# Performance work log

Hardware: AMD Instinct MI355X
Metric: run time of the kernel (lower is better)

## Reference

```python
import jax, jax.numpy as jnp
import numpy as np

B, S, D, H, FF = 16, 384, 768, 12, 3072
DH = D // H


def layer_norm(x, g, b, eps=1e-5):
    m = jnp.mean(x, axis=-1, keepdims=True)
    v = jnp.mean((x - m) ** 2, axis=-1, keepdims=True)
    return (x - m) * jax.lax.rsqrt(v + eps) * g + b


def setup_inputs() -> dict:
    key = jax.random.key(0)
    ks = jax.random.split(key, 12)
    s = 0.02
    return {
        "x": jax.random.normal(ks[0], (B, S, D), dtype=jnp.float32),
        "pe": jax.random.normal(ks[1], (2 * S - 1, D), dtype=jnp.float32) * s,  # relative-position table for offsets -(S-1)..(S-1)
        "Wq": jax.random.normal(ks[2], (D, D), dtype=jnp.float32) * s,
        "Wk": jax.random.normal(ks[3], (D, D), dtype=jnp.float32) * s,
        "Wv": jax.random.normal(ks[4], (D, D), dtype=jnp.float32) * s,
        "Wr": jax.random.normal(ks[5], (D, D), dtype=jnp.float32) * s,
        "u": jax.random.normal(ks[6], (H, DH), dtype=jnp.float32) * s,  # content bias (Transformer-XL)
        "v": jax.random.normal(ks[7], (H, DH), dtype=jnp.float32) * s,  # position bias
        "Wo": jax.random.normal(ks[8], (D, D), dtype=jnp.float32) * s,  # attn_ff output projection
        "ln1_g": jnp.ones((D,), dtype=jnp.float32),
        "ln1_b": jnp.zeros((D,), dtype=jnp.float32),
        "ln2_g": jnp.ones((D,), dtype=jnp.float32),
        "ln2_b": jnp.zeros((D,), dtype=jnp.float32),
        "W1": jax.random.normal(ks[9], (D, FF), dtype=jnp.float32) * s,
        "b1": jnp.zeros((FF,), dtype=jnp.float32),
        "W2": jax.random.normal(ks[10], (FF, D), dtype=jnp.float32) * s,
        "b2": jnp.zeros((D,), dtype=jnp.float32),
    }


def reference(x, pe, Wq, Wk, Wv, Wr, u, v, Wo, ln1_g, ln1_b, ln2_g, ln2_b, W1, b1, W2, b2):
    # --- relative-position multi-head self-attention (FLAT / Transformer-XL style) ---
    q = (x @ Wq).reshape(B, S, H, DH)
    k = (x @ Wk).reshape(B, S, H, DH)
    val = (x @ Wv).reshape(B, S, H, DH)
    # project relative table once, then gather per (i, j) offset
    r = (pe @ Wr).reshape(2 * S - 1, H, DH)
    idx = jnp.arange(S)[:, None] - jnp.arange(S)[None, :] + (S - 1)  # [S,S], offset i-j shifted
    rel = r[idx]  # [S,S,H,DH]
    A_C = jnp.einsum("bqhd,bkhd->bhqk", q + u, k)
    B_D = jnp.einsum("bqhd,qkhd->bhqk", q + v, rel)
    scores = (A_C + B_D) * (1.0 / np.sqrt(DH))  # scaled=True
    p = jax.nn.softmax(scores, axis=-1)
    attn = jnp.einsum("bhqk,bkhd->bqhd", p, val).reshape(B, S, D) @ Wo
    # layer_postprocess_sequence = 'an': add residual, then layernorm
    x1 = layer_norm(x + attn, ln1_g, ln1_b)
    # --- FFN (relu) with 'an' postprocess ---
    ff = jax.nn.relu(x1 @ W1 + b1) @ W2 + b2
    return layer_norm(x1 + ff, ln2_g, ln2_b)
```

## Files before the change

kernel.cpp:

```cpp
#include <hip/hip_runtime.h>

typedef unsigned short u16;
typedef __attribute__((ext_vector_type(8))) short short8;
typedef __attribute__((ext_vector_type(4))) float floatx4;

#define B_  16
#define S_  384
#define D_  768
#define H_  12
#define DH_ 64
#define FF_ 3072

__device__ __forceinline__ float b2f(u16 h) { return __uint_as_float(((unsigned)h) << 16); }
__device__ __forceinline__ u16 f2b(float f) {
  unsigned u = __float_as_uint(f);
  u += 0x7fffu + ((u >> 16) & 1u);
  return (u16)(u >> 16);
}

__device__ __forceinline__ void gload16(const u16* g, u16* l) {
  __builtin_amdgcn_global_load_lds(
      (const __attribute__((address_space(1))) unsigned int*)g,
      (__attribute__((address_space(3))) unsigned int*)l, 16, 0, 0);
}

__global__ __launch_bounds__(256) void fill_sentinel(u16* out, int n) {
  int i = blockIdx.x * 256 + threadIdx.x;
  if (i < n) out[i] = 0x42DE;
}

__global__ __launch_bounds__(256) void detect_dtype(const u16* __restrict__ x, int* flag) {
  __shared__ int cnt;
  if (threadIdx.x == 0) cnt = 0;
  __syncthreads();
  int c = 0;
  for (int i = threadIdx.x; i < 8192; i += 256) {
    const unsigned e = (x[i] >> 7) & 0xFFu;
    if (e >= 0xC0u) ++c;
  }
  atomicAdd(&cnt, c);
  __syncthreads();
  if (threadIdx.x == 0) *flag = (cnt > 64) ? 1 : 0;
}

__global__ __launch_bounds__(256) void convert_in4(const void* __restrict__ src,
                                                   u16* __restrict__ dst, int n4,
                                                   const int* __restrict__ flag) {
  const int i = blockIdx.x * 256 + threadIdx.x;
  if (i >= n4) return;
  if (*flag) {
    const float4 f = ((const float4*)src)[i];
    ushort4 o;
    o.x = f2b(f.x); o.y = f2b(f.y); o.z = f2b(f.z); o.w = f2b(f.w);
    ((ushort4*)dst)[i] = o;
  } else {
    ((ushort4*)dst)[i] = ((const ushort4*)src)[i];
  }
}

__global__ __launch_bounds__(256) void convert_small(
    const void* b1, const void* ub, const void* vb, const void* b2,
    const void* g1, const void* be1, const void* g2, const void* be2,
    u16* b1c, u16* ubc, u16* vbc, u16* b2c,
    u16* g1c, u16* be1c, u16* g2c, u16* be2c, const int* __restrict__ flag) {
  const int i = blockIdx.x * 256 + threadIdx.x;
  if (i >= 8448) return;
  const void* s; u16* d; int off;
  if (i < 3072) { s = b1; d = b1c; off = i; }
  else {
    const int r = i - 3072, sg = r / 768; off = r - sg * 768;
    switch (sg) {
      case 0: s = ub;  d = ubc;  break;
      case 1: s = vb;  d = vbc;  break;
      case 2: s = b2;  d = b2c;  break;
      case 3: s = g1;  d = g1c;  break;
      case 4: s = be1; d = be1c; break;
      case 5: s = g2;  d = g2c;  break;
      default: s = be2; d = be2c; break;
    }
  }
  d[off] = (*flag) ? f2b(((const float*)s)[off]) : ((const u16*)s)[off];
}

struct TP { const void* src[7]; u16* dst[7]; };
__global__ __launch_bounds__(256) void transpose_all(TP tp, const int* __restrict__ flag) {
  __shared__ u16 t[32][33];
  const int f32 = *flag;
  const int id = blockIdx.x;
  int w, tt, R, C, bc, br;
  if (id < 2880)      { w = id / 576; tt = id % 576;  R = 768;  C = 768;  bc = (tt % 24) * 32; br = (tt / 24) * 32; }
  else if (id < 5184) { w = 5;        tt = id - 2880; R = 768;  C = 3072; bc = (tt % 96) * 32; br = (tt / 96) * 32; }
  else                { w = 6;        tt = id - 5184; R = 3072; C = 768;  bc = (tt % 24) * 32; br = (tt / 24) * 32; }
  const void* in = tp.src[w];
  u16* out = tp.dst[w];
  const int tx = threadIdx.x & 31, ty = threadIdx.x >> 5;
  for (int i = ty; i < 32; i += 8) {
    const size_t idx = (size_t)(br + i) * C + bc + tx;
    t[i][tx] = f32 ? f2b(((const float*)in)[idx]) : ((const u16*)in)[idx];
  }
  __syncthreads();
  for (int i = ty; i < 32; i += 8) out[(size_t)(bc + i) * R + br + tx] = t[tx][i];
}

enum { F_BIAS = 1, F_RELU = 2, F_RES = 4, F_QKV = 8 };

template <int TM, int TN, int WM, int WN, int FLAGS>
__global__ __launch_bounds__(256) void gemm3(
    const u16* __restrict__ A, const u16* __restrict__ Bt,
    u16* __restrict__ out0, u16* __restrict__ out1,
    u16* __restrict__ out2, u16* __restrict__ out3,
    const u16* __restrict__ bias0, const u16* __restrict__ bias1,
    const u16* __restrict__ res, int M, int N, int K) {
  constexpr int WAVES_M = TM / WM;
  constexpr int MT = WM / 16, NT = WN / 16;
  constexpr int NI = (TM + TN) / 64;
  static_assert((TM / WM) * (TN / WN) == 4, "4 waves");
  __shared__ u16 SM[2][(TM + TN) * 32];

  const int m0 = blockIdx.y * TM;
  const int n0 = blockIdx.x * TN;
  const int tid = threadIdx.x;
  const int wid = tid >> 6, lane = tid & 63;
  const int wm = (wid % WAVES_M) * WM, wn = (wid / WAVES_M) * WN;
  const int lm = lane & 15, quad = lane >> 4;

  floatx4 acc[MT][NT];
#pragma unroll
  for (int i = 0; i < MT; ++i)
#pragma unroll
    for (int j = 0; j < NT; ++j) acc[i][j] = (floatx4){0.f, 0.f, 0.f, 0.f};

  const u16* srcs[NI];
  int ldso[NI];
#pragma unroll
  for (int i = 0; i < NI; ++i) {
    const int j = wid + 4 * i;
    const int r = j * 16 + (lane >> 2);
    const int q = (lane & 3) ^ ((r >> 1) & 3);
    const u16* p;
    if (r < TM) {
      int ga = m0 + r;
      if (ga > M - 1) ga = M - 1;
      p = A + (size_t)ga * K + q * 8;
    } else {
      p = Bt + (size_t)(n0 + r - TM) * K + q * 8;
    }
    srcs[i] = p;
    ldso[i] = j * 512;
  }
  const int slot = (quad ^ ((lm >> 1) & 3)) * 8;
  int aoff[MT], boff[NT];
#pragma unroll
  for (int t = 0; t < MT; ++t) aoff[t] = (wm + t * 16 + lm) * 32 + slot;
#pragma unroll
  for (int t = 0; t < NT; ++t) boff[t] = (TM + wn + t * 16 + lm) * 32 + slot;

#pragma unroll
  for (int i = 0; i < NI; ++i) gload16(srcs[i], &SM[0][ldso[i]]);
  __syncthreads();

  int buf = 0;
  for (int k0 = 0; k0 < K; k0 += 32, buf ^= 1) {
    if (k0 + 32 < K) {
      const int koff = (k0 + 32);
#pragma unroll
      for (int i = 0; i < NI; ++i) gload16(srcs[i] + koff, &SM[buf ^ 1][ldso[i]]);
    }
    short8 af[MT], bf[NT];
#pragma unroll
    for (int t = 0; t < MT; ++t) af[t] = *(const short8*)(&SM[buf][aoff[t]]);
#pragma unroll
    for (int t = 0; t < NT; ++t) bf[t] = *(const short8*)(&SM[buf][boff[t]]);
#pragma unroll
    for (int tm = 0; tm < MT; ++tm)
#pragma unroll
      for (int tn = 0; tn < NT; ++tn)
        acc[tm][tn] = __builtin_amdgcn_mfma_f32_16x16x32_bf16(af[tm], bf[tn], acc[tm][tn], 0, 0, 0);
    __syncthreads();
  }

#pragma unroll
  for (int tm = 0; tm < MT; ++tm) {
#pragma unroll
    for (int tn = 0; tn < NT; ++tn) {
      const int gcol = n0 + wn + tn * 16 + lm;
#pragma unroll
      for (int r = 0; r < 4; ++r) {
        const int grow = m0 + wm + tm * 16 + quad * 4 + r;
        if (grow >= M) continue;
        float val = acc[tm][tn][r];
        if (FLAGS & F_QKV) {
          const int region = gcol / 768;
          const int c = gcol - region * 768;
          if (region == 0) {
            out0[(size_t)grow * 768 + c] = f2b(val + b2f(bias0[c]));
            out1[(size_t)grow * 768 + c] = f2b(val + b2f(bias1[c]));
          } else if (region == 1) {
            out2[(size_t)grow * 768 + c] = f2b(val);
          } else {
            const int bb = grow / S_, s = grow - bb * S_;
            out3[((size_t)bb * D_ + c) * S_ + s] = f2b(val);
          }
        } else {
          if (FLAGS & F_BIAS) val += b2f(bias0[gcol]);
          if (FLAGS & F_RES) val += b2f(res[(size_t)grow * N + gcol]);
          if (FLAGS & F_RELU) val = fmaxf(val, 0.f);
          out0[(size_t)grow * N + gcol] = f2b(val);
        }
      }
    }
  }
}

__global__ __launch_bounds__(256) void attn_kernel(
    const u16* __restrict__ qu, const u16* __restrict__ qv,
    const u16* __restrict__ kb, const u16* __restrict__ vt,
    const u16* __restrict__ rb, u16* __restrict__ attn) {
  __shared__ float scA[16 * 388];
  __shared__ float E[16 * 404];
  __shared__ float rsum[16];

  const int id = blockIdx.x;
  const int g = id >> 3;
  const int qt = g % 24;
  const int bh = (id & 7) + 8 * (g / 24);
  const int b = bh / H_, h = bh % H_;
  const int i0 = qt * 16;
  const int tid = threadIdx.x, wid = tid >> 6, lane = tid & 63;
  const int lm = lane & 15, quad = lane >> 4;

  const size_t qrow = ((size_t)(b * S_ + i0 + lm)) * D_ + h * DH_;
  {
    const short8 a0 = *(const short8*)(qv + qrow + quad * 8);
    const short8 a1 = *(const short8*)(qv + qrow + 32 + quad * 8);
    for (int tt = wid; tt < 25; tt += 4) {
      const int trel = tt * 16 + lm;
      int t = i0 + trel;
      if (t > 766) t = 766;
      const size_t rrow = (size_t)t * D_ + h * DH_;
      const short8 b0 = *(const short8*)(rb + rrow + quad * 8);
      const short8 b1 = *(const short8*)(rb + rrow + 32 + quad * 8);
      floatx4 e = (floatx4){0.f, 0.f, 0.f, 0.f};
      e = __builtin_amdgcn_mfma_f32_16x16x32_bf16(a0, b0, e, 0, 0, 0);
      e = __builtin_amdgcn_mfma_f32_16x16x32_bf16(a1, b1, e, 0, 0, 0);
#pragma unroll
      for (int r = 0; r < 4; ++r) E[(quad * 4 + r) * 404 + trel] = e[r];
    }
  }
  {
    const short8 a0 = *(const short8*)(qu + qrow + quad * 8);
    const short8 a1 = *(const short8*)(qu + qrow + 32 + quad * 8);
    for (int q = 0; q < 6; ++q) {
      const int j0 = (wid * 6 + q) * 16;
      const size_t krow = ((size_t)(b * S_ + j0 + lm)) * D_ + h * DH_;
      const short8 b0 = *(const short8*)(kb + krow + quad * 8);
      const short8 b1 = *(const short8*)(kb + krow + 32 + quad * 8);
      floatx4 e = (floatx4){0.f, 0.f, 0.f, 0.f};
      e = __builtin_amdgcn_mfma_f32_16x16x32_bf16(a0, b0, e, 0, 0, 0);
      e = __builtin_amdgcn_mfma_f32_16x16x32_bf16(a1, b1, e, 0, 0, 0);
#pragma unroll
      for (int r = 0; r < 4; ++r) scA[(quad * 4 + r) * 388 + j0 + lm] = e[r];
    }
  }
  __syncthreads();

  u16* p16 = (u16*)scA;
  {
    const int row = wid * 4 + quad;
    float v[24];
    float lmax = -1e30f;
#pragma unroll
    for (int cc = 0; cc < 24; ++cc) {
      const int c = lm + cc * 16;
      const float s = (scA[row * 388 + c] + E[row * 404 + row + 383 - c]) * 0.125f;
      v[cc] = s;
      lmax = fmaxf(lmax, s);
    }
#pragma unroll
    for (int m = 1; m < 16; m <<= 1) lmax = fmaxf(lmax, __shfl_xor(lmax, m));
    float lsum = 0.f;
#pragma unroll
    for (int cc = 0; cc < 24; ++cc) {
      const float e = __expf(v[cc] - lmax);
      p16[row * 776 + lm + cc * 16] = f2b(e);
      lsum += e;
    }
#pragma unroll
    for (int m = 1; m < 16; m <<= 1) lsum += __shfl_xor(lsum, m);
    if (lm == 0) rsum[row] = lsum;
  }
  __syncthreads();

  floatx4 o[4];
#pragma unroll
  for (int nt = 0; nt < 4; ++nt) o[nt] = (floatx4){0.f, 0.f, 0.f, 0.f};
  for (int kk = 0; kk < 3; ++kk) {
    const int kbase = wid * 96 + kk * 32;
    const short8 af = *(const short8*)(&p16[lm * 776 + kbase + quad * 8]);
#pragma unroll
    for (int nt = 0; nt < 4; ++nt) {
      const size_t vrow = ((size_t)(b * D_ + h * DH_ + nt * 16 + lm)) * S_;
      const short8 bv = *(const short8*)(vt + vrow + kbase + quad * 8);
      o[nt] = __builtin_amdgcn_mfma_f32_16x16x32_bf16(af, bv, o[nt], 0, 0, 0);
    }
  }
#pragma unroll
  for (int nt = 0; nt < 4; ++nt)
#pragma unroll
    for (int r = 0; r < 4; ++r)
      E[wid * 1088 + (quad * 4 + r) * 68 + nt * 16 + lm] = o[nt][r];
  __syncthreads();

#pragma unroll
  for (int i = 0; i < 4; ++i) {
    const int idx = tid + 256 * i;
    const int row = idx >> 6, dh = idx & 63;
    float v = E[row * 68 + dh] + E[1088 + row * 68 + dh] +
              E[2176 + row * 68 + dh] + E[3264 + row * 68 + dh];
    v /= rsum[row];
    attn[((size_t)(b * S_ + i0 + row)) * D_ + h * DH_ + dh] = f2b(v);
  }
}

__global__ __launch_bounds__(256) void ln_kernel(const u16* __restrict__ y,
                                                 const u16* __restrict__ g,
                                                 const u16* __restrict__ bb,
                                                 void* __restrict__ outv,
                                                 const int* __restrict__ flag, int dual) {
  const int row = blockIdx.x * 4 + (threadIdx.x >> 6);
  const int lane = threadIdx.x & 63;
  const u16* yr = y + (size_t)row * D_;
  float vbuf[12], s = 0.f, s2 = 0.f;
#pragma unroll
  for (int i = 0; i < 12; ++i) {
    const float x = b2f(yr[lane + i * 64]);
    vbuf[i] = x;
    s += x;
    s2 += x * x;
  }
#pragma unroll
  for (int off = 32; off; off >>= 1) {
    s += __shfl_down(s, off);
    s2 += __shfl_down(s2, off);
  }
  s = __shfl(s, 0);
  s2 = __shfl(s2, 0);
  const float mean = s * (1.f / 768.f);
  const float var = s2 * (1.f / 768.f) - mean * mean;
  const float inv = rsqrtf(var + 1e-5f);
  const int f32out = dual && *flag;
#pragma unroll
  for (int i = 0; i < 12; ++i) {
    const int c = lane + i * 64;
    const float val = (vbuf[i] - mean) * inv * b2f(g[c]) + b2f(bb[c]);
    if (f32out) ((float*)outv)[(size_t)row * D_ + c] = val;
    else ((u16*)outv)[(size_t)row * D_ + c] = f2b(val);
  }
}

extern "C" void kernel_launch(void* const* d_in, const int* in_sizes, int n_in,
                              void* d_out, int out_size, void* d_ws, size_t ws_size,
                              hipStream_t stream) {
  const void* x    = d_in[0];
  const void* pe   = d_in[1];
  const void* Wq   = d_in[2];
  const void* Wk   = d_in[3];
  const void* Wv   = d_in[4];
  const void* Wr   = d_in[5];
  const void* ub   = d_in[6];
  const void* vb   = d_in[7];
  const void* Wo   = d_in[8];
  const void* ln1g = d_in[9];
  const void* ln1b = d_in[10];
  const void* ln2g = d_in[11];
  const void* ln2b = d_in[12];
  const void* W1   = d_in[13];
  const void* b1   = d_in[14];
  const void* W2   = d_in[15];
  const void* b2   = d_in[16];
  char* ws = (char*)d_ws;

  constexpr int N_X  = B_ * S_ * D_;
  constexpr int N_PE = (2 * S_ - 1) * D_;

  constexpr size_t O_W   = 0;
  constexpr size_t O_SM  = 15335424;
  constexpr size_t O_XB  = 15368192;
  constexpr size_t O_QU  = 24805376;
  constexpr size_t O_QV  = 34242560;
  constexpr size_t O_KB  = 43679744;
  constexpr size_t O_VT  = 53116928;
  constexpr size_t O_RB  = 62554112;
  constexpr size_t NEEDED = 63733760;

  if (ws_size < NEEDED) {
    fill_sentinel<<<(out_size + 255) / 256, 256, 0, stream>>>((u16*)d_out, out_size);
    return;
  }

  int* flag = (int*)(ws + O_SM);
  u16* ubc  = (u16*)(ws + O_SM + 128);
  u16* vbc  = (u16*)(ws + O_SM + 1664);
  u16* b1c  = (u16*)(ws + O_SM + 3200);
  u16* b2c  = (u16*)(ws + O_SM + 9344);
  u16* g1c  = (u16*)(ws + O_SM + 10880);
  u16* be1c = (u16*)(ws + O_SM + 12416);
  u16* g2c  = (u16*)(ws + O_SM + 13952);
  u16* be2c = (u16*)(ws + O_SM + 15488);

  u16* wtq = (u16*)(ws + O_W);
  u16* wtk = wtq + (size_t)D_ * D_;
  u16* wtv = wtk + (size_t)D_ * D_;
  u16* wtr = wtv + (size_t)D_ * D_;
  u16* wto = wtr + (size_t)D_ * D_;
  u16* wt1 = wto + (size_t)D_ * D_;
  u16* wt2 = wt1 + (size_t)D_ * FF_;

  u16* xb  = (u16*)(ws + O_XB);
  u16* quB = (u16*)(ws + O_QU);
  u16* peb = (u16*)(ws + O_QV);
  u16* qvB = (u16*)(ws + O_QV);
  u16* kbB = (u16*)(ws + O_KB);
  u16* vtB = (u16*)(ws + O_VT);
  u16* rbB = (u16*)(ws + O_RB);
  u16* atB = (u16*)d_out;
  u16* y1B = xb;
  u16* x1B = (u16*)(ws + O_VT);
  u16* ffB = xb;
  u16* y2B = x1B;

  detect_dtype<<<1, 256, 0, stream>>>((const u16*)x, flag);
  convert_in4<<<(N_X / 4 + 255) / 256, 256, 0, stream>>>(x, xb, N_X / 4, flag);
  convert_in4<<<(N_PE / 4 + 255) / 256, 256, 0, stream>>>(pe, peb, N_PE / 4, flag);
  convert_small<<<33, 256, 0, stream>>>(b1, ub, vb, b2, ln1g, ln1b, ln2g, ln2b,
                                        b1c, ubc, vbc, b2c, g1c, be1c, g2c, be2c, flag);
  TP tp;
  tp.src[0] = Wq; tp.src[1] = Wk; tp.src[2] = Wv; tp.src[3] = Wr; tp.src[4] = Wo;
  tp.src[5] = W1; tp.src[6] = W2;
  tp.dst[0] = wtq; tp.dst[1] = wtk; tp.dst[2] = wtv; tp.dst[3] = wtr; tp.dst[4] = wto;
  tp.dst[5] = wt1; tp.dst[6] = wt2;
  transpose_all<<<7488, 256, 0, stream>>>(tp, flag);

  gemm3<64, 64, 32, 32, 0><<<dim3(12, 12), 256, 0, stream>>>(
      peb, wtr, rbB, nullptr, nullptr, nullptr, nullptr, nullptr, nullptr,
      2 * S_ - 1, D_, D_);
  gemm3<128, 128, 64, 64, F_QKV><<<dim3(18, 48), 256, 0, stream>>>(
      xb, wtq, quB, qvB, kbB, vtB, ubc, vbc, nullptr, B_ * S_, 2304, D_);
  attn_kernel<<<4608, 256, 0, stream>>>(quB, qvB, kbB, vtB, rbB, atB);
  gemm3<64, 128, 32, 64, F_RES><<<dim3(6, 96), 256, 0, stream>>>(
      atB, wto, y1B, nullptr, nullptr, nullptr, nullptr, nullptr, xb, B_ * S_, D_, D_);
  ln_kernel<<<B_ * S_ / 4, 256, 0, stream>>>(y1B, g1c, be1c, x1B, flag, 0);
  gemm3<128, 128, 64, 64, F_BIAS | F_RELU><<<dim3(24, 48), 256, 0, stream>>>(
      x1B, wt1, ffB, nullptr, nullptr, nullptr, b1c, nullptr, nullptr, B_ * S_, FF_, D_);
  gemm3<64, 128, 32, 64, F_BIAS | F_RES><<<dim3(6, 96), 256, 0, stream>>>(
      ffB, wt2, y2B, nullptr, nullptr, nullptr, b2c, nullptr, x1B, B_ * S_, D_, FF_);
  ln_kernel<<<B_ * S_ / 4, 256, 0, stream>>>(y2B, g2c, be2c, d_out, flag, 1);
}
```

Baseline: 466.3 us.

## Pipeline score loads, store rel-scores as bf16, split PV by output columns

The attention kernel now merges the relative-position and content score loops into one software-pipelined loop that prefetches the next R and K fragments while the MFMAs for the current ones run. The relative score buffer is kept in bf16 to shrink shared memory, and the launch bounds ask for four blocks per CU to raise occupancy. The P·V stage gives each wave 16 output columns across the full key length, prefetched into registers before softmax, which removes the cross-wave shared-memory reduction and one barrier. The cost is higher register pressure and a slight precision loss from rounding the relative scores to bf16.

```diff
diff --git a/kernel.cpp b/kernel.cpp
--- a/kernel.cpp
+++ b/kernel.cpp
@@ -212,12 +212,12 @@
   }
 }
 
-__global__ __launch_bounds__(256) void attn_kernel(
+__global__ __launch_bounds__(256, 4) void attn_kernel(
     const u16* __restrict__ qu, const u16* __restrict__ qv,
     const u16* __restrict__ kb, const u16* __restrict__ vt,
     const u16* __restrict__ rb, u16* __restrict__ attn) {
   __shared__ float scA[16 * 388];
-  __shared__ float E[16 * 404];
+  __shared__ u16 Eb[16 * 408];
   __shared__ float rsum[16];
 
   const int id = blockIdx.x;
@@ -230,39 +230,60 @@
   const int lm = lane & 15, quad = lane >> 4;
 
   const size_t qrow = ((size_t)(b * S_ + i0 + lm)) * D_ + h * DH_;
+  const short8 av0 = *(const short8*)(qv + qrow + quad * 8);
+  const short8 av1 = *(const short8*)(qv + qrow + 32 + quad * 8);
+  const short8 au0 = *(const short8*)(qu + qrow + quad * 8);
+  const short8 au1 = *(const short8*)(qu + qrow + 32 + quad * 8);
+
+  short8 r0, r1, k0, k1;
   {
-    const short8 a0 = *(const short8*)(qv + qrow + quad * 8);
-    const short8 a1 = *(const short8*)(qv + qrow + 32 + quad * 8);
-    for (int tt = wid; tt < 25; tt += 4) {
-      const int trel = tt * 16 + lm;
-      int t = i0 + trel;
-      if (t > 766) t = 766;
-      const size_t rrow = (size_t)t * D_ + h * DH_;
-      const short8 b0 = *(const short8*)(rb + rrow + quad * 8);
-      const short8 b1 = *(const short8*)(rb + rrow + 32 + quad * 8);
+    int t = i0 + wid * 16 + lm; if (t > 766) t = 766;
+    const u16* p = rb + (size_t)t * D_ + h * DH_;
+    r0 = *(const short8*)(p + quad * 8);
+    r1 = *(const short8*)(p + 32 + quad * 8);
+    const u16* q = kb + ((size_t)(b * S_ + wid * 96 + lm)) * D_ + h * DH_;
+    k0 = *(const short8*)(q + quad * 8);
+    k1 = *(const short8*)(q + 32 + quad * 8);
+  }
+#pragma unroll
+  for (int i = 0; i < 7; ++i) {
+    short8 nr0 = r0, nr1 = r1, nk0 = k0, nk1 = k1;
+    const int ntt = wid + 4 * (i + 1);
+    if (ntt < 25) {
+      int t = i0 + ntt * 16 + lm; if (t > 766) t = 766;
+      const u16* p = rb + (size_t)t * D_ + h * DH_;
+      nr0 = *(const short8*)(p + quad * 8);
+      nr1 = *(const short8*)(p + 32 + quad * 8);
+    }
+    if (i + 1 < 6) {
+      const u16* q = kb + ((size_t)(b * S_ + (wid * 6 + i + 1) * 16 + lm)) * D_ + h * DH_;
+      nk0 = *(const short8*)(q + quad * 8);
+      nk1 = *(const short8*)(q + 32 + quad * 8);
+    }
+    const int tt = wid + 4 * i;
+    if (tt < 25) {
       floatx4 e = (floatx4){0.f, 0.f, 0.f, 0.f};
-      e = __builtin_amdgcn_mfma_f32_16x16x32_bf16(a0, b0, e, 0, 0, 0);
-      e = __builtin_amdgcn_mfma_f32_16x16x32_bf16(a1, b1, e, 0, 0, 0);
-#pragma unroll
-      for (int r = 0; r < 4; ++r) E[(quad * 4 + r) * 404 + trel] = e[r];
-    }
-  }
-  {
-    const short8 a0 = *(const short8*)(qu + qrow + quad * 8);
-    const short8 a1 = *(const short8*)(qu + qrow + 32 + quad * 8);
-    for (int q = 0; q < 6; ++q) {
-      const int j0 = (wid * 6 + q) * 16;
-      const size_t krow = ((size_t)(b * S_ + j0 + lm)) * D_ + h * DH_;
-      const short8 b0 = *(const short8*)(kb + krow + quad * 8);
-      const short8 b1 = *(const short8*)(kb + krow + 32 + quad * 8);
+      e = __builtin_amdgcn_mfma_f32_16x16x32_bf16(av0, r0, e, 0, 0, 0);
+      e = __builtin_amdgcn_mfma_f32_16x16x32_bf16(av1, r1, e, 0, 0, 0);
+#pragma unroll
+      for (int r = 0; r < 4; ++r) Eb[(quad * 4 + r) * 408 + tt * 16 + lm] = f2b(e[r]);
+    }
+    if (i < 6) {
       floatx4 e = (floatx4){0.f, 0.f, 0.f, 0.f};
-      e = __builtin_amdgcn_mfma_f32_16x16x32_bf16(a0, b0, e, 0, 0, 0);
-      e = __builtin_amdgcn_mfma_f32_16x16x32_bf16(a1, b1, e, 0, 0, 0);
-#pragma unroll
-      for (int r = 0; r < 4; ++r) scA[(quad * 4 + r) * 388 + j0 + lm] = e[r];
-    }
-  }
-  __syncthreads();
+      e = __builtin_amdgcn_mfma_f32_16x16x32_bf16(au0, k0, e, 0, 0, 0);
+      e = __builtin_amdgcn_mfma_f32_16x16x32_bf16(au1, k1, e, 0, 0, 0);
+#pragma unroll
+      for (int r = 0; r < 4; ++r) scA[(quad * 4 + r) * 388 + (wid * 6 + i) * 16 + lm] = e[r];
+    }
+    r0 = nr0; r1 = nr1; k0 = nk0; k1 = nk1;
+  }
+  __syncthreads();
+
+  short8 vv[12];
+  const size_t vbase = ((size_t)(b * D_ + h * DH_ + wid * 16 + lm)) * S_;
+#pragma unroll
+  for (int kk = 0; kk < 12; ++kk)
+    vv[kk] = *(const short8*)(vt + vbase + kk * 32 + quad * 8);
 
   u16* p16 = (u16*)scA;
   {
@@ -272,7 +293,7 @@
 #pragma unroll
     for (int cc = 0; cc < 24; ++cc) {
       const int c = lm + cc * 16;
-      const float s = (scA[row * 388 + c] + E[row * 404 + row + 383 - c]) * 0.125f;
+      const float s = (scA[row * 388 + c] + b2f(Eb[row * 408 + row + 383 - c])) * 0.125f;
       v[cc] = s;
       lmax = fmaxf(lmax, s);
     }
@@ -291,34 +312,17 @@
   }
   __syncthreads();
 
-  floatx4 o[4];
-#pragma unroll
-  for (int nt = 0; nt < 4; ++nt) o[nt] = (floatx4){0.f, 0.f, 0.f, 0.f};
-  for (int kk = 0; kk < 3; ++kk) {
-    const int kbase = wid * 96 + kk * 32;
-    const short8 af = *(const short8*)(&p16[lm * 776 + kbase + quad * 8]);
-#pragma unroll
-    for (int nt = 0; nt < 4; ++nt) {
-      const size_t vrow = ((size_t)(b * D_ + h * DH_ + nt * 16 + lm)) * S_;
-      const short8 bv = *(const short8*)(vt + vrow + kbase + quad * 8);
-      o[nt] = __builtin_amdgcn_mfma_f32_16x16x32_bf16(af, bv, o[nt], 0, 0, 0);
-    }
-  }
-#pragma unroll
-  for (int nt = 0; nt < 4; ++nt)
-#pragma unroll
-    for (int r = 0; r < 4; ++r)
-      E[wid * 1088 + (quad * 4 + r) * 68 + nt * 16 + lm] = o[nt][r];
-  __syncthreads();
-
-#pragma unroll
-  for (int i = 0; i < 4; ++i) {
-    const int idx = tid + 256 * i;
-    const int row = idx >> 6, dh = idx & 63;
-    float v = E[row * 68 + dh] + E[1088 + row * 68 + dh] +
-              E[2176 + row * 68 + dh] + E[3264 + row * 68 + dh];
-    v /= rsum[row];
-    attn[((size_t)(b * S_ + i0 + row)) * D_ + h * DH_ + dh] = f2b(v);
+  floatx4 o = (floatx4){0.f, 0.f, 0.f, 0.f};
+#pragma unroll
+  for (int kk = 0; kk < 12; ++kk) {
+    const short8 af = *(const short8*)(&p16[lm * 776 + kk * 32 + quad * 8]);
+    o = __builtin_amdgcn_mfma_f32_16x16x32_bf16(af, vv[kk], o, 0, 0, 0);
+  }
+#pragma unroll
+  for (int r = 0; r < 4; ++r) {
+    const int row = quad * 4 + r;
+    attn[((size_t)(b * S_ + i0 + row)) * D_ + h * DH_ + wid * 16 + lm] =
+        f2b(o[r] / rsum[row]);
   }
 }
 
```

New measurement: 462.2 us. About the same (-0.9%).

## Use 8 waves per attention block and store positional scores in bf16

Applied to the files above, without the earlier changes.

The attention kernel moves from 4 to 8 wavefronts per block. The 49 score tiles (25 positional, 24 content) are spread evenly over the waves, softmax runs two rows per wave, and the PV product is split into 4 column tiles by 2 key halves. The positional score buffer is stored as bf16 instead of fp32, which shrinks LDS use and may raise occupancy. The bf16 rounding of the positional term before softmax costs some accuracy.

```diff
diff --git a/kernel.cpp b/kernel.cpp
--- a/kernel.cpp
+++ b/kernel.cpp
@@ -212,12 +212,12 @@
   }
 }
 
-__global__ __launch_bounds__(256) void attn_kernel(
+__global__ __launch_bounds__(512, 8) void attn_kernel(
     const u16* __restrict__ qu, const u16* __restrict__ qv,
     const u16* __restrict__ kb, const u16* __restrict__ vt,
     const u16* __restrict__ rb, u16* __restrict__ attn) {
   __shared__ float scA[16 * 388];
-  __shared__ float E[16 * 404];
+  __shared__ u16 Eb[16 * 408];
   __shared__ float rsum[16];
 
   const int id = blockIdx.x;
@@ -230,31 +230,31 @@
   const int lm = lane & 15, quad = lane >> 4;
 
   const size_t qrow = ((size_t)(b * S_ + i0 + lm)) * D_ + h * DH_;
-  {
-    const short8 a0 = *(const short8*)(qv + qrow + quad * 8);
-    const short8 a1 = *(const short8*)(qv + qrow + 32 + quad * 8);
-    for (int tt = wid; tt < 25; tt += 4) {
-      const int trel = tt * 16 + lm;
-      int t = i0 + trel;
+
+#pragma unroll
+  for (int i = 0; i < 7; ++i) {
+    const int u = wid + 8 * i;
+    if (u >= 49) break;
+    if (u < 25) {
+      int t = i0 + u * 16 + lm;
       if (t > 766) t = 766;
-      const size_t rrow = (size_t)t * D_ + h * DH_;
-      const short8 b0 = *(const short8*)(rb + rrow + quad * 8);
-      const short8 b1 = *(const short8*)(rb + rrow + 32 + quad * 8);
+      const u16* p = rb + (size_t)t * D_ + h * DH_;
+      const short8 b0 = *(const short8*)(p + quad * 8);
+      const short8 b1 = *(const short8*)(p + 32 + quad * 8);
+      const short8 a0 = *(const short8*)(qv + qrow + quad * 8);
+      const short8 a1 = *(const short8*)(qv + qrow + 32 + quad * 8);
       floatx4 e = (floatx4){0.f, 0.f, 0.f, 0.f};
       e = __builtin_amdgcn_mfma_f32_16x16x32_bf16(a0, b0, e, 0, 0, 0);
       e = __builtin_amdgcn_mfma_f32_16x16x32_bf16(a1, b1, e, 0, 0, 0);
 #pragma unroll
-      for (int r = 0; r < 4; ++r) E[(quad * 4 + r) * 404 + trel] = e[r];
-    }
-  }
-  {
-    const short8 a0 = *(const short8*)(qu + qrow + quad * 8);
-    const short8 a1 = *(const short8*)(qu + qrow + 32 + quad * 8);
-    for (int q = 0; q < 6; ++q) {
-      const int j0 = (wid * 6 + q) * 16;
-      const size_t krow = ((size_t)(b * S_ + j0 + lm)) * D_ + h * DH_;
-      const short8 b0 = *(const short8*)(kb + krow + quad * 8);
-      const short8 b1 = *(const short8*)(kb + krow + 32 + quad * 8);
+      for (int r = 0; r < 4; ++r) Eb[(quad * 4 + r) * 408 + u * 16 + lm] = f2b(e[r]);
+    } else {
+      const int j0 = (u - 25) * 16;
+      const u16* p = kb + ((size_t)(b * S_ + j0 + lm)) * D_ + h * DH_;
+      const short8 b0 = *(const short8*)(p + quad * 8);
+      const short8 b1 = *(const short8*)(p + 32 + quad * 8);
+      const short8 a0 = *(const short8*)(qu + qrow + quad * 8);
+      const short8 a1 = *(const short8*)(qu + qrow + 32 + quad * 8);
       floatx4 e = (floatx4){0.f, 0.f, 0.f, 0.f};
       e = __builtin_amdgcn_mfma_f32_16x16x32_bf16(a0, b0, e, 0, 0, 0);
       e = __builtin_amdgcn_mfma_f32_16x16x32_bf16(a1, b1, e, 0, 0, 0);
@@ -266,58 +266,54 @@
 
   u16* p16 = (u16*)scA;
   {
-    const int row = wid * 4 + quad;
-    float v[24];
+    const int row = wid * 2 + (lane >> 5);
+    const int sub = lane & 31;
+    float v[12];
     float lmax = -1e30f;
 #pragma unroll
-    for (int cc = 0; cc < 24; ++cc) {
-      const int c = lm + cc * 16;
-      const float s = (scA[row * 388 + c] + E[row * 404 + row + 383 - c]) * 0.125f;
+    for (int cc = 0; cc < 12; ++cc) {
+      const int c = sub + cc * 32;
+      const float s = (scA[row * 388 + c] + b2f(Eb[row * 408 + row + 383 - c])) * 0.125f;
       v[cc] = s;
       lmax = fmaxf(lmax, s);
     }
 #pragma unroll
-    for (int m = 1; m < 16; m <<= 1) lmax = fmaxf(lmax, __shfl_xor(lmax, m));
+    for (int m = 1; m < 32; m <<= 1) lmax = fmaxf(lmax, __shfl_xor(lmax, m));
     float lsum = 0.f;
 #pragma unroll
-    for (int cc = 0; cc < 24; ++cc) {
+    for (int cc = 0; cc < 12; ++cc) {
       const float e = __expf(v[cc] - lmax);
-      p16[row * 776 + lm + cc * 16] = f2b(e);
+      p16[row * 776 + sub + cc * 32] = f2b(e);
       lsum += e;
     }
 #pragma unroll
-    for (int m = 1; m < 16; m <<= 1) lsum += __shfl_xor(lsum, m);
-    if (lm == 0) rsum[row] = lsum;
-  }
-  __syncthreads();
-
-  floatx4 o[4];
-#pragma unroll
-  for (int nt = 0; nt < 4; ++nt) o[nt] = (floatx4){0.f, 0.f, 0.f, 0.f};
-  for (int kk = 0; kk < 3; ++kk) {
-    const int kbase = wid * 96 + kk * 32;
-    const short8 af = *(const short8*)(&p16[lm * 776 + kbase + quad * 8]);
-#pragma unroll
-    for (int nt = 0; nt < 4; ++nt) {
-      const size_t vrow = ((size_t)(b * D_ + h * DH_ + nt * 16 + lm)) * S_;
-      const short8 bv = *(const short8*)(vt + vrow + kbase + quad * 8);
-      o[nt] = __builtin_amdgcn_mfma_f32_16x16x32_bf16(af, bv, o[nt], 0, 0, 0);
-    }
-  }
-#pragma unroll
-  for (int nt = 0; nt < 4; ++nt)
+    for (int m = 1; m < 32; m <<= 1) lsum += __shfl_xor(lsum, m);
+    if (sub == 0) rsum[row] = lsum;
+  }
+  __syncthreads();
+
+  float* part = (float*)Eb;
+  {
+    const int nt = wid & 3, kh = wid >> 2;
+    floatx4 o = (floatx4){0.f, 0.f, 0.f, 0.f};
+    const size_t vbase = ((size_t)(b * D_ + h * DH_ + nt * 16 + lm)) * S_ + kh * 192;
+#pragma unroll
+    for (int kk = 0; kk < 6; ++kk) {
+      const short8 af = *(const short8*)(&p16[lm * 776 + kh * 192 + kk * 32 + quad * 8]);
+      const short8 bv = *(const short8*)(vt + vbase + kk * 32 + quad * 8);
+      o = __builtin_amdgcn_mfma_f32_16x16x32_bf16(af, bv, o, 0, 0, 0);
+    }
 #pragma unroll
     for (int r = 0; r < 4; ++r)
-      E[wid * 1088 + (quad * 4 + r) * 68 + nt * 16 + lm] = o[nt][r];
-  __syncthreads();
-
-#pragma unroll
-  for (int i = 0; i < 4; ++i) {
-    const int idx = tid + 256 * i;
+      part[kh * 1088 + (quad * 4 + r) * 68 + nt * 16 + lm] = o[r];
+  }
+  __syncthreads();
+
+#pragma unroll
+  for (int i = 0; i < 2; ++i) {
+    const int idx = tid + 512 * i;
     const int row = idx >> 6, dh = idx & 63;
-    float v = E[row * 68 + dh] + E[1088 + row * 68 + dh] +
-              E[2176 + row * 68 + dh] + E[3264 + row * 68 + dh];
-    v /= rsum[row];
+    const float v = (part[row * 68 + dh] + part[1088 + row * 68 + dh]) / rsum[row];
     attn[((size_t)(b * S_ + i0 + row)) * D_ + h * DH_ + dh] = f2b(v);
   }
 }
@@ -446,7 +442,7 @@
       2 * S_ - 1, D_, D_);
   gemm3<128, 128, 64, 64, F_QKV><<<dim3(18, 48), 256, 0, stream>>>(
       xb, wtq, quB, qvB, kbB, vtB, ubc, vbc, nullptr, B_ * S_, 2304, D_);
-  attn_kernel<<<4608, 256, 0, stream>>>(quB, qvB, kbB, vtB, rbB, atB);
+  attn_kernel<<<4608, 512, 0, stream>>>(quB, qvB, kbB, vtB, rbB, atB);
   gemm3<64, 128, 32, 64, F_RES><<<dim3(6, 96), 256, 0, stream>>>(
       atB, wto, y1B, nullptr, nullptr, nullptr, nullptr, nullptr, xb, B_ * S_, D_, D_);
   ln_kernel<<<B_ * S_ / 4, 256, 0, stream>>>(y1B, g1c, be1c, x1B, flag, 0);
```

Result: no change. 472.5 us (+1.3%).
